# Performance work log

Measured on AMD Instinct MI355X. Metric: run time of the kernel, lower is better.

Reference implementation:

```python
import jax, jax.numpy as jnp
import numpy as np

N_EMBD = 64
BLOCK = 8
HEADS = 4
HS = N_EMBD // HEADS  # 16
EPS = 1e-5


def layernorm(x, g, b):
    mu = jnp.mean(x, axis=-1, keepdims=True)
    var = jnp.var(x, axis=-1, keepdims=True)
    return (x - mu) * jax.lax.rsqrt(var + EPS) * g + b


def setup_inputs() -> dict:
    key = jax.random.key(0)
    ks = jax.random.split(key, 12)
    B = 65536
    s = 0.02
    return {
        "x": jax.random.normal(ks[0], (B, BLOCK, N_EMBD), dtype=jnp.float32),
        # per-head Q/K/V projections stacked: [H, C, hs]
        "Wq": jax.random.normal(ks[1], (HEADS, N_EMBD, HS), dtype=jnp.float32) * s,
        "Wk": jax.random.normal(ks[2], (HEADS, N_EMBD, HS), dtype=jnp.float32) * s,
        "Wv": jax.random.normal(ks[3], (HEADS, N_EMBD, HS), dtype=jnp.float32) * s,
        "Wp": jax.random.normal(ks[4], (N_EMBD, N_EMBD), dtype=jnp.float32) * s,
        "bp": jnp.zeros((N_EMBD,), dtype=jnp.float32),
        "W1": jax.random.normal(ks[5], (N_EMBD, 4 * N_EMBD), dtype=jnp.float32) * s,
        "b1": jnp.zeros((4 * N_EMBD,), dtype=jnp.float32),
        "W2": jax.random.normal(ks[6], (4 * N_EMBD, N_EMBD), dtype=jnp.float32) * s,
        "b2": jnp.zeros((N_EMBD,), dtype=jnp.float32),
        "g1": jnp.ones((N_EMBD,), dtype=jnp.float32),
        "beta1": jnp.zeros((N_EMBD,), dtype=jnp.float32),
        "g2": jnp.ones((N_EMBD,), dtype=jnp.float32),
        "beta2": jnp.zeros((N_EMBD,), dtype=jnp.float32),
    }


def reference(x, Wq, Wk, Wv, Wp, bp, W1, b1, W2, b2, g1, beta1, g2, beta2):
    B, T, C = x.shape
    # --- pre-LN self-attention ---
    h = layernorm(x, g1, beta1)
    q = jnp.einsum('btc,hcd->bhtd', h, Wq)
    k = jnp.einsum('btc,hcd->bhtd', h, Wk)
    v = jnp.einsum('btc,hcd->bhtd', h, Wv)
    # NOTE: original scales by n_embd**-0.5 (C of the input), not head_size
    wei = jnp.einsum('bhtd,bhsd->bhts', q, k) * (C ** -0.5)
    tril = jnp.tril(jnp.ones((T, T), dtype=bool))
    wei = jnp.where(tril, wei, -jnp.inf)
    wei = jax.nn.softmax(wei, axis=-1)  # dropout off (eval mode)
    attn = jnp.einsum('bhts,bhsd->bhtd', wei, v)
    attn = attn.transpose(0, 2, 1, 3).reshape(B, T, C)  # concat heads
    sa = attn @ Wp + bp
    x = x + sa
    # --- pre-LN MLP ---
    h2 = layernorm(x, g2, beta2)
    ff = jax.nn.relu(h2 @ W1 + b1) @ W2 + b2
    return x + ff
```

## Files before the change

kernel.cpp:

```cpp
#include <hip/hip_runtime.h>
#include <hip/hip_bf16.h>
#include <stdint.h>

typedef __attribute__((ext_vector_type(8))) short bf16x8;
typedef __attribute__((ext_vector_type(4))) float f32x4;


static __device__ __forceinline__ unsigned short f2bf(float f) {
    union { __hip_bfloat16 h; unsigned short u; } cv;
    cv.h = __float2bfloat16(f);
    return cv.u;
}
static __device__ __forceinline__ unsigned int f2bf2(float a, float b) {
    return (unsigned int)f2bf(a) | ((unsigned int)f2bf(b) << 16);
}
static __device__ __forceinline__ bf16x8 mk8(uint2 a, uint2 b) {
    union { uint4 u; bf16x8 v; } c;
    c.u = make_uint4(a.x, a.y, b.x, b.y);
    return c.v;
}
static __device__ __forceinline__ uint2 packbf(f32x4 a) {
    return make_uint2(f2bf2(a[0], a[1]), f2bf2(a[2], a[3]));
}
static __device__ __forceinline__ uint2 lnq(f32x4 x, float mu, float inv, f32x4 g, f32x4 b) {
    return make_uint2(f2bf2((x[0]-mu)*inv*g[0]+b[0], (x[1]-mu)*inv*g[1]+b[1]),
                      f2bf2((x[2]-mu)*inv*g[2]+b[2], (x[3]-mu)*inv*g[3]+b[3]));
}
static __device__ __forceinline__ uint2 relupack0(f32x4 a) {
    return make_uint2(f2bf2(fmaxf(a[0],0.f), fmaxf(a[1],0.f)),
                      f2bf2(fmaxf(a[2],0.f), fmaxf(a[3],0.f)));
}

#define MFMA(A,B,C) __builtin_amdgcn_mfma_f32_16x16x32_bf16((A),(B),(C),0,0,0)
#define SB() __builtin_amdgcn_sched_barrier(0)

static __device__ __forceinline__ uint2 attn_tail(f32x4 sa, uint2 vw, int fr, int fg) {
    const f32x4 zf = {0.f,0.f,0.f,0.f};
    const uint2 z2 = make_uint2(0u,0u);
    int tk0 = 4*fg, frq = fr & 7;
    bool v8 = ((fr ^ tk0) & 8) == 0;
    float p0 = (v8 && (((tk0+0)&7) <= frq)) ? __expf(sa[0]*0.125f) : 0.f;
    float p1 = (v8 && (((tk0+1)&7) <= frq)) ? __expf(sa[1]*0.125f) : 0.f;
    float p2 = (v8 && (((tk0+2)&7) <= frq)) ? __expf(sa[2]*0.125f) : 0.f;
    float p3 = (v8 && (((tk0+3)&7) <= frq)) ? __expf(sa[3]*0.125f) : 0.f;
    float rsum = p0 + p1 + p2 + p3;
    rsum += __shfl_xor(rsum, 16, 64);
    rsum += __shfl_xor(rsum, 32, 64);
    float pinv = __builtin_amdgcn_rcpf(rsum);
    uint2 pb = make_uint2(f2bf2(p0,p1), f2bf2(p2,p3));
    f32x4 oa = MFMA(mk8(vw, z2), mk8(pb, z2), zf);
    return make_uint2(f2bf2(oa[0]*pinv, oa[1]*pinv), f2bf2(oa[2]*pinv, oa[3]*pinv));
}

static __device__ __forceinline__ void attn_head2(
    bf16x8 wq0, bf16x8 wq1, bf16x8 wk0, bf16x8 wk1, bf16x8 wv0, bf16x8 wv1,
    bf16x8 hA0, bf16x8 hA1, bf16x8 hB0, bf16x8 hB1, int fr, int fg,
    uint2& oA, uint2& oB)
{
    const f32x4 zf = {0.f,0.f,0.f,0.f};
    const uint2 z2 = make_uint2(0u,0u);
    {
        f32x4 qa = MFMA(wq0, hA0, zf); qa = MFMA(wq1, hA1, qa);
        f32x4 ka = MFMA(wk0, hA0, zf); ka = MFMA(wk1, hA1, ka);
        f32x4 va = MFMA(hA0, wv0, zf); va = MFMA(hA1, wv1, va);
        uint2 qw = packbf(qa), kw = packbf(ka), vw = packbf(va);
        f32x4 sa = MFMA(mk8(kw, z2), mk8(qw, z2), zf);
        oA = attn_tail(sa, vw, fr, fg);
    }
    {
        f32x4 qa = MFMA(wq0, hB0, zf); qa = MFMA(wq1, hB1, qa);
        f32x4 ka = MFMA(wk0, hB0, zf); ka = MFMA(wk1, hB1, ka);
        f32x4 va = MFMA(hB0, wv0, zf); va = MFMA(hB1, wv1, va);
        uint2 qw = packbf(qa), kw = packbf(ka), vw = packbf(va);
        f32x4 sa = MFMA(mk8(kw, z2), mk8(qw, z2), zf);
        oB = attn_tail(sa, vw, fr, fg);
    }
}

__global__ __launch_bounds__(512)
void pack_weights(const float* __restrict__ Wq, const float* __restrict__ Wk,
                  const float* __restrict__ Wv, const float* __restrict__ Wp,
                  const float* __restrict__ W1, const float* __restrict__ W2,
                  const float* __restrict__ bp, const float* __restrict__ b1,
                  const float* __restrict__ b2, const float* __restrict__ g1,
                  const float* __restrict__ be1, const float* __restrict__ g2,
                  const float* __restrict__ be2, unsigned short* __restrict__ gw)
{
    int e = blockIdx.x * 512 + threadIdx.x;
    if (e < 49152) {
        int j = e & 7, ln = (e >> 3) & 63, f = e >> 9;
        int fr_ = ln & 15, fg_ = ln >> 4;
        int u = j >> 2, r_ = j & 3;
        float src;
        if (f < 24) {
            int sel = f >> 3, hd = (f >> 1) & 3, m = f & 1;
            int c = 16*(2*m + u) + 4*fg_ + r_;
            const float* W = (sel == 0) ? Wq : ((sel == 1) ? Wk : Wv);
            src = W[hd*1024 + c*16 + fr_];
        } else if (f < 32) {
            int t = f - 24, nt = t >> 1, m = t & 1;
            int d = 16*(2*m + u) + 4*fg_ + r_;
            src = Wp[d*64 + 16*nt + fr_];
        } else if (f < 64) {
            int t = f - 32, tt = t >> 1, m = t & 1;
            int c = 16*(2*m + u) + 4*fg_ + r_;
            src = W1[c*256 + 16*tt + fr_];
        } else {
            int t = f - 64, nt = t >> 3, m = t & 7;
            int n1 = 16*(2*m + u) + 4*fg_ + r_;
            src = W2[n1*64 + 16*nt + fr_];
        }
        gw[e] = f2bf(src);
    } else {
        int t = e - 49152;
        if (t < 640) {
            float v;
            if      (t < 64)  v = g1[t];
            else if (t < 128) v = be1[t - 64];
            else if (t < 192) v = g2[t - 128];
            else if (t < 256) v = be2[t - 192];
            else if (t < 320) v = bp[t - 256];
            else if (t < 384) v = b2[t - 320];
            else              v = b1[t - 384];
            ((float*)(gw + 49152))[t] = v;
        }
    }
}

__global__ __launch_bounds__(512, 1)
void fused_block(const unsigned short* __restrict__ gw,
                 const float* __restrict__ xg, float* __restrict__ out,
                 int nPairsTotal)
{
    __shared__ __align__(16) unsigned char LDS[68096];

    const int tid  = threadIdx.x;
    const int lane = tid & 63;
    const int wid  = tid >> 6;
    const int fr   = lane & 15;
    const int fg   = lane >> 4;

    {
        const uint4* src = (const uint4*)gw;
        uint4* dst = (uint4*)LDS;
        #pragma unroll
        for (int k = 0; k < 8; ++k)
            dst[tid + 512*k] = src[tid + 512*k];
        if (tid < 160) dst[tid + 4096] = src[tid + 6144];
    }
    __syncthreads();

    const float* PG = (const float*)(LDS + 65536);
    #define WFL(F) (*(const bf16x8*)(LDS + ((F) << 10) + (lane << 4)))
    #define W2G(F) (*(const bf16x8*)(gw + ((F) << 9) + (lane << 3)))
    #define PG4(I) (*(const f32x4*)(PG + (I) + 4*fg))

    const int pipe = blockIdx.x * 8 + wid;
    const f32x4 zf = {0.f, 0.f, 0.f, 0.f};
    const int xoff = fr*64 + 4*fg;
    const int nP2 = nPairsTotal >> 1;

    #pragma unroll 1
    for (int gp2 = pipe; gp2 < nP2; gp2 += 4096) {
        const float* xb = xg + (size_t)gp2 * 2048;
        float*      obp = out + (size_t)gp2 * 2048;

        f32x4 xA0 = *(const f32x4*)(xb + xoff);
        f32x4 xA1 = *(const f32x4*)(xb + xoff + 16);
        f32x4 xA2 = *(const f32x4*)(xb + xoff + 32);
        f32x4 xA3 = *(const f32x4*)(xb + xoff + 48);
        f32x4 xB0 = *(const f32x4*)(xb + 1024 + xoff);
        f32x4 xB1 = *(const f32x4*)(xb + 1024 + xoff + 16);
        f32x4 xB2 = *(const f32x4*)(xb + 1024 + xoff + 32);
        f32x4 xB3 = *(const f32x4*)(xb + 1024 + xoff + 48);
        SB();

        #define ACC4(S,SS,V) { S += V[0]+V[1]+V[2]+V[3]; \
                               SS += V[0]*V[0]+V[1]*V[1]+V[2]*V[2]+V[3]*V[3]; }

        bf16x8 hA0, hA1, hB0, hB1;
        {
            float sA=0.f, qA=0.f, sB=0.f, qB=0.f;
            ACC4(sA,qA,xA0); ACC4(sA,qA,xA1); ACC4(sA,qA,xA2); ACC4(sA,qA,xA3);
            ACC4(sB,qB,xB0); ACC4(sB,qB,xB1); ACC4(sB,qB,xB2); ACC4(sB,qB,xB3);
            sA += __shfl_xor(sA,16,64); qA += __shfl_xor(qA,16,64);
            sA += __shfl_xor(sA,32,64); qA += __shfl_xor(qA,32,64);
            sB += __shfl_xor(sB,16,64); qB += __shfl_xor(qB,16,64);
            sB += __shfl_xor(sB,32,64); qB += __shfl_xor(qB,32,64);
            float muA = sA*0.015625f, invA = rsqrtf(qA*0.015625f - muA*muA + 1e-5f);
            float muB = sB*0.015625f, invB = rsqrtf(qB*0.015625f - muB*muB + 1e-5f);
            hA0 = mk8(lnq(xA0,muA,invA,PG4(0),  PG4(64)),
                      lnq(xA1,muA,invA,PG4(16), PG4(80)));
            hA1 = mk8(lnq(xA2,muA,invA,PG4(32), PG4(96)),
                      lnq(xA3,muA,invA,PG4(48), PG4(112)));
            hB0 = mk8(lnq(xB0,muB,invB,PG4(0),  PG4(64)),
                      lnq(xB1,muB,invB,PG4(16), PG4(80)));
            hB1 = mk8(lnq(xB2,muB,invB,PG4(32), PG4(96)),
                      lnq(xB3,muB,invB,PG4(48), PG4(112)));
        }
        SB();

        uint2 oA0,oA1,oA2,oA3, oB0,oB1,oB2,oB3;
        attn_head2(WFL(0), WFL(1), WFL(8),  WFL(9),  WFL(16), WFL(17),
                   hA0,hA1, hB0,hB1, fr, fg, oA0, oB0);
        attn_head2(WFL(2), WFL(3), WFL(10), WFL(11), WFL(18), WFL(19),
                   hA0,hA1, hB0,hB1, fr, fg, oA1, oB1);
        SB();
        attn_head2(WFL(4), WFL(5), WFL(12), WFL(13), WFL(20), WFL(21),
                   hA0,hA1, hB0,hB1, fr, fg, oA2, oB2);
        attn_head2(WFL(6), WFL(7), WFL(14), WFL(15), WFL(22), WFL(23),
                   hA0,hA1, hB0,hB1, fr, fg, oA3, oB3);
        SB();

        {
            bf16x8 olo = mk8(oA0,oA1), ohi = mk8(oA2,oA3);
            bf16x8 plo = mk8(oB0,oB1), phi = mk8(oB2,oB3);
            #define PROJ(NT, XA, XB) { \
                f32x4 bv = PG4(256 + 16*(NT)); \
                f32x4 ca, cb; \
                ca[0]=XA[0]+bv[0]; ca[1]=XA[1]+bv[1]; ca[2]=XA[2]+bv[2]; ca[3]=XA[3]+bv[3]; \
                cb[0]=XB[0]+bv[0]; cb[1]=XB[1]+bv[1]; cb[2]=XB[2]+bv[2]; cb[3]=XB[3]+bv[3]; \
                bf16x8 wp0 = WFL(24+(NT)*2+0), wp1 = WFL(24+(NT)*2+1); \
                f32x4 pa = MFMA(wp0, olo, ca); pa = MFMA(wp1, ohi, pa); \
                f32x4 pb = MFMA(wp0, plo, cb); pb = MFMA(wp1, phi, pb); \
                XA = pa; XB = pb; }
            PROJ(0, xA0, xB0); PROJ(1, xA1, xB1); PROJ(2, xA2, xB2); PROJ(3, xA3, xB3);
            #undef PROJ
        }
        SB();

        bf16x8 cA0, cA1, cB0, cB1;
        f32x4 fA0, fA1, fA2, fA3, fB0, fB1, fB2, fB3;
        {
            float sA=0.f, qA=0.f, sB=0.f, qB=0.f;
            ACC4(sA,qA,xA0); ACC4(sA,qA,xA1); ACC4(sA,qA,xA2); ACC4(sA,qA,xA3);
            ACC4(sB,qB,xB0); ACC4(sB,qB,xB1); ACC4(sB,qB,xB2); ACC4(sB,qB,xB3);
            sA += __shfl_xor(sA,16,64); qA += __shfl_xor(qA,16,64);
            sA += __shfl_xor(sA,32,64); qA += __shfl_xor(qA,32,64);
            sB += __shfl_xor(sB,16,64); qB += __shfl_xor(qB,16,64);
            sB += __shfl_xor(sB,32,64); qB += __shfl_xor(qB,32,64);
            float muA = sA*0.015625f, invA = rsqrtf(qA*0.015625f - muA*muA + 1e-5f);
            float muB = sB*0.015625f, invB = rsqrtf(qB*0.015625f - muB*muB + 1e-5f);
            cA0 = mk8(lnq(xA0,muA,invA,PG4(128), PG4(192)),
                      lnq(xA1,muA,invA,PG4(144), PG4(208)));
            cA1 = mk8(lnq(xA2,muA,invA,PG4(160), PG4(224)),
                      lnq(xA3,muA,invA,PG4(176), PG4(240)));
            cB0 = mk8(lnq(xB0,muB,invB,PG4(128), PG4(192)),
                      lnq(xB1,muB,invB,PG4(144), PG4(208)));
            cB1 = mk8(lnq(xB2,muB,invB,PG4(160), PG4(224)),
                      lnq(xB3,muB,invB,PG4(176), PG4(240)));
            #define FINIT(NT, FA, FB, XA, XB) { \
                f32x4 bv = PG4(320 + 16*(NT)); \
                FA[0]=XA[0]+bv[0]; FA[1]=XA[1]+bv[1]; FA[2]=XA[2]+bv[2]; FA[3]=XA[3]+bv[3]; \
                FB[0]=XB[0]+bv[0]; FB[1]=XB[1]+bv[1]; FB[2]=XB[2]+bv[2]; FB[3]=XB[3]+bv[3]; }
            FINIT(0, fA0, fB0, xA0, xB0); FINIT(1, fA1, fB1, xA1, xB1);
            FINIT(2, fA2, fB2, xA2, xB2); FINIT(3, fA3, fB3, xA3, xB3);
            #undef FINIT
        }
        SB();

        #pragma unroll 1
        for (int m2 = 0; m2 < 8; ++m2) {
            bf16x8 w20 = W2G(64 + 0*8 + m2);
            bf16x8 w21 = W2G(64 + 1*8 + m2);
            bf16x8 w22 = W2G(64 + 2*8 + m2);
            bf16x8 w23 = W2G(64 + 3*8 + m2);
            int t0 = 2*m2, t1 = 2*m2 + 1;
            bf16x8 w10 = WFL(32+t0*2+0), w11 = WFL(32+t0*2+1);
            f32x4 bi0 = PG4(384 + 16*t0);
            f32x4 aA = MFMA(w10, cA0, bi0); aA = MFMA(w11, cA1, aA);
            f32x4 aB = MFMA(w10, cB0, bi0); aB = MFMA(w11, cB1, aB);
            uint2 frA0 = relupack0(aA), frB0 = relupack0(aB);
            bf16x8 w12 = WFL(32+t1*2+0), w13 = WFL(32+t1*2+1);
            f32x4 bi1 = PG4(384 + 16*t1);
            f32x4 cAa = MFMA(w12, cA0, bi1); cAa = MFMA(w13, cA1, cAa);
            f32x4 cBa = MFMA(w12, cB0, bi1); cBa = MFMA(w13, cB1, cBa);
            uint2 frA1 = relupack0(cAa), frB1 = relupack0(cBa);
            bf16x8 ffrA = mk8(frA0, frA1), ffrB = mk8(frB0, frB1);
            fA0 = MFMA(w20, ffrA, fA0); fB0 = MFMA(w20, ffrB, fB0);
            fA1 = MFMA(w21, ffrA, fA1); fB1 = MFMA(w21, ffrB, fB1);
            fA2 = MFMA(w22, ffrA, fA2); fB2 = MFMA(w22, ffrB, fB2);
            fA3 = MFMA(w23, ffrA, fA3); fB3 = MFMA(w23, ffrB, fB3);
        }

        *(f32x4*)(obp + xoff)             = fA0;
        *(f32x4*)(obp + xoff + 16)        = fA1;
        *(f32x4*)(obp + xoff + 32)        = fA2;
        *(f32x4*)(obp + xoff + 48)        = fA3;
        *(f32x4*)(obp + 1024 + xoff)      = fB0;
        *(f32x4*)(obp + 1024 + xoff + 16) = fB1;
        *(f32x4*)(obp + 1024 + xoff + 32) = fB2;
        *(f32x4*)(obp + 1024 + xoff + 48) = fB3;
        #undef ACC4
    }
    #undef WFL
    #undef W2G
    #undef PG4
}

extern "C" void kernel_launch(void* const* d_in, const int* in_sizes, int n_in,
                              void* d_out, int out_size, void* d_ws, size_t ws_size,
                              hipStream_t stream) {
    const float* x   = (const float*)d_in[0];
    const float* Wq  = (const float*)d_in[1];
    const float* Wk  = (const float*)d_in[2];
    const float* Wv  = (const float*)d_in[3];
    const float* Wp  = (const float*)d_in[4];
    const float* bp  = (const float*)d_in[5];
    const float* W1  = (const float*)d_in[6];
    const float* b1  = (const float*)d_in[7];
    const float* W2  = (const float*)d_in[8];
    const float* b2  = (const float*)d_in[9];
    const float* g1  = (const float*)d_in[10];
    const float* be1 = (const float*)d_in[11];
    const float* g2  = (const float*)d_in[12];
    const float* be2 = (const float*)d_in[13];
    unsigned short* gw = (unsigned short*)d_ws;

    pack_weights<<<dim3(98), dim3(512), 0, stream>>>(
        Wq, Wk, Wv, Wp, W1, W2, bp, b1, b2, g1, be1, g2, be2, gw);

    int nPairs = in_sizes[0] / 1024;
    fused_block<<<dim3(512), dim3(512), 0, stream>>>(
        gw, x, (float*)d_out, nPairs);
}
```

Measured before the change: 106.8 us.

## Stage proj/MLP weights in LDS and stream QKV weights from global with prefetch

```diff
diff --git a/kernel.cpp b/kernel.cpp
--- a/kernel.cpp
+++ b/kernel.cpp
@@ -127,12 +127,12 @@
     }
 }
 
-__global__ __launch_bounds__(512, 1)
+__global__ __launch_bounds__(512, 2)
 void fused_block(const unsigned short* __restrict__ gw,
                  const float* __restrict__ xg, float* __restrict__ out,
                  int nPairsTotal)
 {
-    __shared__ __align__(16) unsigned char LDS[68096];
+    __shared__ __align__(16) unsigned char LDS[76288];
 
     const int tid  = threadIdx.x;
     const int lane = tid & 63;
@@ -144,16 +144,16 @@
         const uint4* src = (const uint4*)gw;
         uint4* dst = (uint4*)LDS;
         #pragma unroll
-        for (int k = 0; k < 8; ++k)
-            dst[tid + 512*k] = src[tid + 512*k];
-        if (tid < 160) dst[tid + 4096] = src[tid + 6144];
+        for (int k = 0; k < 9; ++k)
+            dst[tid + 512*k] = src[1536 + tid + 512*k];
+        if (tid < 160) dst[4608 + tid] = src[6144 + tid];
     }
     __syncthreads();
 
-    const float* PG = (const float*)(LDS + 65536);
-    #define WFL(F) (*(const bf16x8*)(LDS + ((F) << 10) + (lane << 4)))
-    #define W2G(F) (*(const bf16x8*)(gw + ((F) << 9) + (lane << 3)))
-    #define PG4(I) (*(const f32x4*)(PG + (I) + 4*fg))
+    const float* PG = (const float*)(LDS + 73728);
+    #define WFS(F)  (*(const bf16x8*)(LDS + (((F) - 24) << 10) + (lane << 4)))
+    #define QKVG(F) (*(const bf16x8*)(gw + ((F) << 9) + (lane << 3)))
+    #define PG4(I)  (*(const f32x4*)(PG + (I) + 4*fg))
 
     const int pipe = blockIdx.x * 8 + wid;
     const f32x4 zf = {0.f, 0.f, 0.f, 0.f};
@@ -173,6 +173,9 @@
         f32x4 xB1 = *(const f32x4*)(xb + 1024 + xoff + 16);
         f32x4 xB2 = *(const f32x4*)(xb + 1024 + xoff + 32);
         f32x4 xB3 = *(const f32x4*)(xb + 1024 + xoff + 48);
+        bf16x8 aq0 = QKVG(0),  aq1 = QKVG(1);
+        bf16x8 ak0 = QKVG(8),  ak1 = QKVG(9);
+        bf16x8 av0 = QKVG(16), av1 = QKVG(17);
         SB();
 
         #define ACC4(S,SS,V) { S += V[0]+V[1]+V[2]+V[3]; \
@@ -198,18 +201,21 @@
             hB1 = mk8(lnq(xB2,muB,invB,PG4(32), PG4(96)),
                       lnq(xB3,muB,invB,PG4(48), PG4(112)));
         }
-        SB();
 
         uint2 oA0,oA1,oA2,oA3, oB0,oB1,oB2,oB3;
-        attn_head2(WFL(0), WFL(1), WFL(8),  WFL(9),  WFL(16), WFL(17),
-                   hA0,hA1, hB0,hB1, fr, fg, oA0, oB0);
-        attn_head2(WFL(2), WFL(3), WFL(10), WFL(11), WFL(18), WFL(19),
-                   hA0,hA1, hB0,hB1, fr, fg, oA1, oB1);
-        SB();
-        attn_head2(WFL(4), WFL(5), WFL(12), WFL(13), WFL(20), WFL(21),
-                   hA0,hA1, hB0,hB1, fr, fg, oA2, oB2);
-        attn_head2(WFL(6), WFL(7), WFL(14), WFL(15), WFL(22), WFL(23),
-                   hA0,hA1, hB0,hB1, fr, fg, oA3, oB3);
+        bf16x8 bq0 = QKVG(2),  bq1 = QKVG(3);
+        bf16x8 bk0 = QKVG(10), bk1 = QKVG(11);
+        bf16x8 bv0 = QKVG(18), bv1 = QKVG(19);
+        attn_head2(aq0,aq1, ak0,ak1, av0,av1, hA0,hA1, hB0,hB1, fr, fg, oA0, oB0);
+        aq0 = QKVG(4);  aq1 = QKVG(5);
+        ak0 = QKVG(12); ak1 = QKVG(13);
+        av0 = QKVG(20); av1 = QKVG(21);
+        attn_head2(bq0,bq1, bk0,bk1, bv0,bv1, hA0,hA1, hB0,hB1, fr, fg, oA1, oB1);
+        bq0 = QKVG(6);  bq1 = QKVG(7);
+        bk0 = QKVG(14); bk1 = QKVG(15);
+        bv0 = QKVG(22); bv1 = QKVG(23);
+        attn_head2(aq0,aq1, ak0,ak1, av0,av1, hA0,hA1, hB0,hB1, fr, fg, oA2, oB2);
+        attn_head2(bq0,bq1, bk0,bk1, bv0,bv1, hA0,hA1, hB0,hB1, fr, fg, oA3, oB3);
         SB();
 
         {
@@ -220,7 +226,7 @@
                 f32x4 ca, cb; \
                 ca[0]=XA[0]+bv[0]; ca[1]=XA[1]+bv[1]; ca[2]=XA[2]+bv[2]; ca[3]=XA[3]+bv[3]; \
                 cb[0]=XB[0]+bv[0]; cb[1]=XB[1]+bv[1]; cb[2]=XB[2]+bv[2]; cb[3]=XB[3]+bv[3]; \
-                bf16x8 wp0 = WFL(24+(NT)*2+0), wp1 = WFL(24+(NT)*2+1); \
+                bf16x8 wp0 = WFS(24+(NT)*2+0), wp1 = WFS(24+(NT)*2+1); \
                 f32x4 pa = MFMA(wp0, olo, ca); pa = MFMA(wp1, ohi, pa); \
                 f32x4 pb = MFMA(wp0, plo, cb); pb = MFMA(wp1, phi, pb); \
                 XA = pa; XB = pb; }
@@ -261,25 +267,25 @@
 
         #pragma unroll 1
         for (int m2 = 0; m2 < 8; ++m2) {
-            bf16x8 w20 = W2G(64 + 0*8 + m2);
-            bf16x8 w21 = W2G(64 + 1*8 + m2);
-            bf16x8 w22 = W2G(64 + 2*8 + m2);
-            bf16x8 w23 = W2G(64 + 3*8 + m2);
             int t0 = 2*m2, t1 = 2*m2 + 1;
-            bf16x8 w10 = WFL(32+t0*2+0), w11 = WFL(32+t0*2+1);
+            bf16x8 w10 = WFS(32+t0*2+0), w11 = WFS(32+t0*2+1);
             f32x4 bi0 = PG4(384 + 16*t0);
             f32x4 aA = MFMA(w10, cA0, bi0); aA = MFMA(w11, cA1, aA);
             f32x4 aB = MFMA(w10, cB0, bi0); aB = MFMA(w11, cB1, aB);
             uint2 frA0 = relupack0(aA), frB0 = relupack0(aB);
-            bf16x8 w12 = WFL(32+t1*2+0), w13 = WFL(32+t1*2+1);
+            bf16x8 w12 = WFS(32+t1*2+0), w13 = WFS(32+t1*2+1);
             f32x4 bi1 = PG4(384 + 16*t1);
             f32x4 cAa = MFMA(w12, cA0, bi1); cAa = MFMA(w13, cA1, cAa);
             f32x4 cBa = MFMA(w12, cB0, bi1); cBa = MFMA(w13, cB1, cBa);
             uint2 frA1 = relupack0(cAa), frB1 = relupack0(cBa);
             bf16x8 ffrA = mk8(frA0, frA1), ffrB = mk8(frB0, frB1);
+            bf16x8 w20 = WFS(64 + 0*8 + m2);
             fA0 = MFMA(w20, ffrA, fA0); fB0 = MFMA(w20, ffrB, fB0);
+            bf16x8 w21 = WFS(64 + 1*8 + m2);
             fA1 = MFMA(w21, ffrA, fA1); fB1 = MFMA(w21, ffrB, fB1);
+            bf16x8 w22 = WFS(64 + 2*8 + m2);
             fA2 = MFMA(w22, ffrA, fA2); fB2 = MFMA(w22, ffrB, fB2);
+            bf16x8 w23 = WFS(64 + 3*8 + m2);
             fA3 = MFMA(w23, ffrA, fA3); fB3 = MFMA(w23, ffrB, fB3);
         }
 
@@ -293,8 +299,8 @@
         *(f32x4*)(obp + 1024 + xoff + 48) = fB3;
         #undef ACC4
     }
-    #undef WFL
-    #undef W2G
+    #undef WFS
+    #undef QKVG
     #undef PG4
 }
 
```

After: 102.7 us. 3.8% less time.
